# Kernel optimization log

Measured on AMD Instinct MI355X. Metric: run time of the kernel, lower is better.

The kernel has to match this reference:

```python
import jax, jax.numpy as jnp
import numpy as np

HIDDEN = 256
BATCH = 16
SEQ = 8192


def setup_inputs() -> dict:
    key = jax.random.key(0)
    k1, k2 = jax.random.split(key)
    x = jax.random.normal(k1, (BATCH, SEQ, HIDDEN), dtype=jnp.float32)
    # rotor_net parameters: Linear(hidden, hidden) followed by tanh
    W = jax.random.normal(k2, (HIDDEN, HIDDEN), dtype=jnp.float32) / np.sqrt(HIDDEN)
    b = jnp.zeros((HIDDEN,), dtype=jnp.float32)
    return {"x": x, "W": W, "b": b}


def reference(x, W, b):
    # Original torch code loops over subseq_size=10 chunks of the flattened
    # (B*S, H) tokens, applying rotor_net to each chunk and concatenating.
    # rotor_net is row-wise (Linear + tanh), so chunked application is
    # mathematically identical to one batched application over all tokens.
    B, S, H = x.shape
    flat = x.reshape(-1, H)                      # (B*S, H)
    out = jnp.tanh(flat @ W.T + b)               # (B*S, H)
    return out.reshape(B, S, -1)
```

## Files before the change

### kernel.cpp

```cpp
#include <hip/hip_runtime.h>
#include <hip/hip_bf16.h>


#define HIDDEN 256
#define M_TOTAL (16 * 8192)
#define NBLK 512
#define CHUNKS_PER_BLK ((M_TOTAL / 32) / NBLK)

using bf16x8 = __attribute__((ext_vector_type(8))) __bf16;
using bf16x4 = __attribute__((ext_vector_type(4))) __bf16;
using f32x4  = __attribute__((ext_vector_type(4))) float;

__device__ __forceinline__ bf16x4 cvt4(float4 v) {
    bf16x4 r;
    r[0] = (__bf16)v.x; r[1] = (__bf16)v.y;
    r[2] = (__bf16)v.z; r[3] = (__bf16)v.w;
    return r;
}

__global__ __launch_bounds__(256) void wfrag_kernel(const float* __restrict__ W,
                                                    __bf16* __restrict__ WF) {
    const int gid  = blockIdx.x * 256 + threadIdx.x;
    const int lane = gid & 63;
    const int t    = (gid >> 6) & 3;
    const int c    = (gid >> 8) & 7;
    const int nb   = gid >> 11;
    const int lr = lane & 15, q = lane >> 4;
    const float* src = W + (size_t)(nb * 64 + t * 16 + lr) * HIDDEN + c * 32 + q * 8;
    float4 lo = *(const float4*)src;
    float4 hi = *(const float4*)(src + 4);
    bf16x8 v;
    v[0] = (__bf16)lo.x; v[1] = (__bf16)lo.y; v[2] = (__bf16)lo.z; v[3] = (__bf16)lo.w;
    v[4] = (__bf16)hi.x; v[5] = (__bf16)hi.y; v[6] = (__bf16)hi.z; v[7] = (__bf16)hi.w;
    *(bf16x8*)(WF + (size_t)gid * 8) = v;
}

__global__ __launch_bounds__(256, 2) void rotor_kernel(const float* __restrict__ X,
                                                       const __bf16* __restrict__ WF,
                                                       const float* __restrict__ bias,
                                                       float* __restrict__ Y) {
    __shared__ __align__(16) unsigned char lds_raw[2 * 16384 + 4 * 4352];
    __bf16* sXb = (__bf16*)lds_raw;
    float*  sO  = (float*)(lds_raw + 32768 + (threadIdx.x >> 6) * 4352);

    const int tid  = threadIdx.x;
    const int lane = tid & 63;
    const int wave = tid >> 6;
    const int lr = lane & 15, q = lane >> 4;

    const int xrow = tid >> 3;
    const int xc   = tid & 7;
    int woff[8];
#pragma unroll
    for (int j = 0; j < 8; ++j)
        woff[j] = j * 1024 + (xrow >> 4) * 512 + ((xc >> 1) * 16 + (xrow & 15)) * 8 + (xc & 1) * 4;

    const size_t blk_row0 = (size_t)blockIdx.x * (CHUNKS_PER_BLK * 32);
    const float* xbase = X + (blk_row0 + xrow) * HIDDEN + xc * 4;

    float4 xr[8];
#pragma unroll
    for (int j = 0; j < 8; ++j) xr[j] = *(const float4*)(xbase + j * 32);

    const __bf16* wf = WF + (size_t)wave * (8 * 4 * 512) + lane * 8;
    bf16x8 bW[8][4];
#pragma unroll
    for (int c = 0; c < 8; ++c)
#pragma unroll
        for (int t = 0; t < 4; ++t)
            bW[c][t] = *(const bf16x8*)(wf + (c * 4 + t) * 512);

    float bv[4];
#pragma unroll
    for (int t = 0; t < 4; ++t) bv[t] = bias[wave * 64 + t * 16 + lr];

#pragma unroll
    for (int j = 0; j < 8; ++j) *(bf16x4*)(sXb + woff[j]) = cvt4(xr[j]);
    asm volatile("s_waitcnt lgkmcnt(0)" ::: "memory");
    __builtin_amdgcn_s_barrier();
    asm volatile("" ::: "memory");

#pragma unroll 1
    for (int it = 0; it < CHUNKS_PER_BLK; ++it) {
        const int cur = it & 1;

        if (it + 1 < CHUNKS_PER_BLK) {
            const float* xs = xbase + (size_t)(it + 1) * 32 * HIDDEN;
#pragma unroll
            for (int j = 0; j < 8; ++j) xr[j] = *(const float4*)(xs + j * 32);
        }

        f32x4 acc[2][4];
#pragma unroll
        for (int m = 0; m < 2; ++m)
#pragma unroll
            for (int t = 0; t < 4; ++t)
                acc[m][t] = (f32x4){0.f, 0.f, 0.f, 0.f};

        const __bf16* sX = sXb + cur * 8192;
#pragma unroll
        for (int c = 0; c < 8; ++c) {
            const __bf16* ab = sX + c * 1024 + lane * 8;
            bf16x8 a0 = *(const bf16x8*)ab;
            bf16x8 a1 = *(const bf16x8*)(ab + 512);
            acc[0][0] = __builtin_amdgcn_mfma_f32_16x16x32_bf16(a0, bW[c][0], acc[0][0], 0, 0, 0);
            acc[0][1] = __builtin_amdgcn_mfma_f32_16x16x32_bf16(a0, bW[c][1], acc[0][1], 0, 0, 0);
            acc[0][2] = __builtin_amdgcn_mfma_f32_16x16x32_bf16(a0, bW[c][2], acc[0][2], 0, 0, 0);
            acc[0][3] = __builtin_amdgcn_mfma_f32_16x16x32_bf16(a0, bW[c][3], acc[0][3], 0, 0, 0);
            acc[1][0] = __builtin_amdgcn_mfma_f32_16x16x32_bf16(a1, bW[c][0], acc[1][0], 0, 0, 0);
            acc[1][1] = __builtin_amdgcn_mfma_f32_16x16x32_bf16(a1, bW[c][1], acc[1][1], 0, 0, 0);
            acc[1][2] = __builtin_amdgcn_mfma_f32_16x16x32_bf16(a1, bW[c][2], acc[1][2], 0, 0, 0);
            acc[1][3] = __builtin_amdgcn_mfma_f32_16x16x32_bf16(a1, bW[c][3], acc[1][3], 0, 0, 0);
        }

        float* yb = Y + (blk_row0 + (size_t)it * 32) * HIDDEN + wave * 64;
#pragma unroll
        for (int m = 0; m < 2; ++m) {
#pragma unroll
            for (int t = 0; t < 4; ++t)
#pragma unroll
                for (int r = 0; r < 4; ++r) {
                    float z = acc[m][t][r] + bv[t];
                    z = fminf(fmaxf(z, -10.f), 10.f);
                    const float e2 = __expf(2.0f * z);
                    sO[(q * 4 + r) * 68 + t * 16 + lr] = __fdividef(e2 - 1.0f, e2 + 1.0f);
                }
#pragma unroll
            for (int j = 0; j < 4; ++j) {
                f32x4 v = *(const f32x4*)(sO + (j * 4 + q) * 68 + lr * 4);
                __builtin_nontemporal_store(v,
                    (f32x4*)(yb + (size_t)(m * 16 + j * 4 + q) * HIDDEN + lr * 4));
            }
        }

        if (it + 1 < CHUNKS_PER_BLK) {
            __bf16* sW = sXb + (cur ^ 1) * 8192;
#pragma unroll
            for (int j = 0; j < 8; ++j) *(bf16x4*)(sW + woff[j]) = cvt4(xr[j]);
        }
        asm volatile("s_waitcnt lgkmcnt(0)" ::: "memory");
        __builtin_amdgcn_s_barrier();
        asm volatile("" ::: "memory");
    }
}

extern "C" void kernel_launch(void* const* d_in, const int* in_sizes, int n_in,
                              void* d_out, int out_size, void* d_ws, size_t ws_size,
                              hipStream_t stream) {
    const float* X    = (const float*)d_in[0];
    const float* W    = (const float*)d_in[1];
    const float* bias = (const float*)d_in[2];
    float* Y          = (float*)d_out;
    __bf16* WF        = (__bf16*)d_ws;

    wfrag_kernel<<<dim3(32), dim3(256), 0, stream>>>(W, WF);
    rotor_kernel<<<dim3(NBLK), dim3(256), 0, stream>>>(X, WF, bias, Y);
}
```

Before: 246.8 us.

## Stream X into swizzled fp32 LDS via direct global-to-LDS loads, split N across blocks

Rows of X are now copied straight from global memory into a double-buffered, XOR-swizzled fp32 LDS tile with global_load_lds, and converted to bf16 only when MFMA operands are read. Register staging and the separate LDS output transpose go away. Each block now handles 16 rows by 128 output columns, so pairs of blocks share input rows. The grid becomes a grid-stride loop of 768 blocks at occupancy 3. The costs are reading each X row twice (relying on L2 reuse between paired blocks) and writing outputs with scalar nontemporal stores instead of 16-byte vector stores.

After: 249.4 us. Within noise of the previous version (+1.1%).

```diff
diff --git a/kernel.cpp b/kernel.cpp
--- a/kernel.cpp
+++ b/kernel.cpp
@@ -4,18 +4,16 @@
 
 #define HIDDEN 256
 #define M_TOTAL (16 * 8192)
-#define NBLK 512
-#define CHUNKS_PER_BLK ((M_TOTAL / 32) / NBLK)
+#define UNITS 16384
+#define NBLK 768
 
 using bf16x8 = __attribute__((ext_vector_type(8))) __bf16;
-using bf16x4 = __attribute__((ext_vector_type(4))) __bf16;
 using f32x4  = __attribute__((ext_vector_type(4))) float;
 
-__device__ __forceinline__ bf16x4 cvt4(float4 v) {
-    bf16x4 r;
-    r[0] = (__bf16)v.x; r[1] = (__bf16)v.y;
-    r[2] = (__bf16)v.z; r[3] = (__bf16)v.w;
-    return r;
+__device__ __forceinline__ void gload16(const void* g, void* l) {
+    __builtin_amdgcn_global_load_lds(
+        (const __attribute__((address_space(1))) void*)g,
+        (__attribute__((address_space(3))) void*)l, 16, 0, 0);
 }
 
 __global__ __launch_bounds__(256) void wfrag_kernel(const float* __restrict__ W,
@@ -35,112 +33,99 @@
     *(bf16x8*)(WF + (size_t)gid * 8) = v;
 }
 
-__global__ __launch_bounds__(256, 2) void rotor_kernel(const float* __restrict__ X,
+__global__ __launch_bounds__(256, 3) void rotor_kernel(const float* __restrict__ X,
                                                        const __bf16* __restrict__ WF,
                                                        const float* __restrict__ bias,
                                                        float* __restrict__ Y) {
-    __shared__ __align__(16) unsigned char lds_raw[2 * 16384 + 4 * 4352];
-    __bf16* sXb = (__bf16*)lds_raw;
-    float*  sO  = (float*)(lds_raw + 32768 + (threadIdx.x >> 6) * 4352);
+    __shared__ __align__(16) float sX[2][16 * 256];
 
     const int tid  = threadIdx.x;
     const int lane = tid & 63;
     const int wave = tid >> 6;
     const int lr = lane & 15, q = lane >> 4;
+    const int bid = blockIdx.x;
+    const int h   = bid & 1;
 
-    const int xrow = tid >> 3;
-    const int xc   = tid & 7;
-    int woff[8];
-#pragma unroll
-    for (int j = 0; j < 8; ++j)
-        woff[j] = j * 1024 + (xrow >> 4) * 512 + ((xc >> 1) * 16 + (xrow & 15)) * 8 + (xc & 1) * 4;
-
-    const size_t blk_row0 = (size_t)blockIdx.x * (CHUNKS_PER_BLK * 32);
-    const float* xbase = X + (blk_row0 + xrow) * HIDDEN + xc * 4;
-
-    float4 xr[8];
-#pragma unroll
-    for (int j = 0; j < 8; ++j) xr[j] = *(const float4*)(xbase + j * 32);
-
-    const __bf16* wf = WF + (size_t)wave * (8 * 4 * 512) + lane * 8;
-    bf16x8 bW[8][4];
+    const int nb  = h * 2 + (wave >> 1);
+    const int tl0 = (wave & 1) * 2;
+    const __bf16* wf = WF + (size_t)nb * (8 * 4 * 512) + lane * 8;
+    bf16x8 bW[8][2];
 #pragma unroll
     for (int c = 0; c < 8; ++c)
 #pragma unroll
-        for (int t = 0; t < 4; ++t)
-            bW[c][t] = *(const bf16x8*)(wf + (c * 4 + t) * 512);
+        for (int t = 0; t < 2; ++t)
+            bW[c][t] = *(const bf16x8*)(wf + (c * 4 + tl0 + t) * 512);
 
-    float bv[4];
+    float bv[2];
 #pragma unroll
-    for (int t = 0; t < 4; ++t) bv[t] = bias[wave * 64 + t * 16 + lr];
+    for (int t = 0; t < 2; ++t) bv[t] = bias[h * 128 + wave * 32 + t * 16 + lr];
 
+    int srcoff[4];
 #pragma unroll
-    for (int j = 0; j < 8; ++j) *(bf16x4*)(sXb + woff[j]) = cvt4(xr[j]);
-    asm volatile("s_waitcnt lgkmcnt(0)" ::: "memory");
+    for (int k = 0; k < 4; ++k) {
+        const int r = wave * 4 + k;
+        srcoff[k] = (lane * 16) ^ (((r & 7) << 5) | ((r & 8) << 1));
+    }
+    const int swr = ((lr & 7) << 3) | ((lr & 8) >> 1);
+
+    {
+        const int rc = bid >> 1;
+#pragma unroll
+        for (int k = 0; k < 4; ++k)
+            gload16((const char*)X + (size_t)(rc * 16 + wave * 4 + k) * 1024 + srcoff[k],
+                    (char*)&sX[0][(wave * 4 + k) * 256]);
+    }
+    asm volatile("s_waitcnt vmcnt(0)" ::: "memory");
     __builtin_amdgcn_s_barrier();
     asm volatile("" ::: "memory");
 
+    int cur = 0;
 #pragma unroll 1
-    for (int it = 0; it < CHUNKS_PER_BLK; ++it) {
-        const int cur = it & 1;
+    for (int u = bid; u < UNITS; u += NBLK) {
+        const int rc = u >> 1;
 
-        if (it + 1 < CHUNKS_PER_BLK) {
-            const float* xs = xbase + (size_t)(it + 1) * 32 * HIDDEN;
+        const int un = u + NBLK;
+        if (un < UNITS) {
+            const int rcn = un >> 1;
 #pragma unroll
-            for (int j = 0; j < 8; ++j) xr[j] = *(const float4*)(xs + j * 32);
+            for (int k = 0; k < 4; ++k)
+                gload16((const char*)X + (size_t)(rcn * 16 + wave * 4 + k) * 1024 + srcoff[k],
+                        (char*)&sX[cur ^ 1][(wave * 4 + k) * 256]);
         }
 
-        f32x4 acc[2][4];
-#pragma unroll
-        for (int m = 0; m < 2; ++m)
-#pragma unroll
-            for (int t = 0; t < 4; ++t)
-                acc[m][t] = (f32x4){0.f, 0.f, 0.f, 0.f};
-
-        const __bf16* sX = sXb + cur * 8192;
+        const float* sxr = &sX[cur][lr * 256];
+        f32x4 acc0 = {0.f, 0.f, 0.f, 0.f};
+        f32x4 acc1 = {0.f, 0.f, 0.f, 0.f};
 #pragma unroll
         for (int c = 0; c < 8; ++c) {
-            const __bf16* ab = sX + c * 1024 + lane * 8;
-            bf16x8 a0 = *(const bf16x8*)ab;
-            bf16x8 a1 = *(const bf16x8*)(ab + 512);
-            acc[0][0] = __builtin_amdgcn_mfma_f32_16x16x32_bf16(a0, bW[c][0], acc[0][0], 0, 0, 0);
-            acc[0][1] = __builtin_amdgcn_mfma_f32_16x16x32_bf16(a0, bW[c][1], acc[0][1], 0, 0, 0);
-            acc[0][2] = __builtin_amdgcn_mfma_f32_16x16x32_bf16(a0, bW[c][2], acc[0][2], 0, 0, 0);
-            acc[0][3] = __builtin_amdgcn_mfma_f32_16x16x32_bf16(a0, bW[c][3], acc[0][3], 0, 0, 0);
-            acc[1][0] = __builtin_amdgcn_mfma_f32_16x16x32_bf16(a1, bW[c][0], acc[1][0], 0, 0, 0);
-            acc[1][1] = __builtin_amdgcn_mfma_f32_16x16x32_bf16(a1, bW[c][1], acc[1][1], 0, 0, 0);
-            acc[1][2] = __builtin_amdgcn_mfma_f32_16x16x32_bf16(a1, bW[c][2], acc[1][2], 0, 0, 0);
-            acc[1][3] = __builtin_amdgcn_mfma_f32_16x16x32_bf16(a1, bW[c][3], acc[1][3], 0, 0, 0);
+            const int b0 = c * 32 + q * 8;
+            f32x4 lo = *(const f32x4*)(sxr + (b0 ^ swr));
+            f32x4 hi = *(const f32x4*)(sxr + ((b0 + 4) ^ swr));
+            bf16x8 a;
+            a[0] = (__bf16)lo[0]; a[1] = (__bf16)lo[1];
+            a[2] = (__bf16)lo[2]; a[3] = (__bf16)lo[3];
+            a[4] = (__bf16)hi[0]; a[5] = (__bf16)hi[1];
+            a[6] = (__bf16)hi[2]; a[7] = (__bf16)hi[3];
+            acc0 = __builtin_amdgcn_mfma_f32_16x16x32_bf16(a, bW[c][0], acc0, 0, 0, 0);
+            acc1 = __builtin_amdgcn_mfma_f32_16x16x32_bf16(a, bW[c][1], acc1, 0, 0, 0);
         }
 
-        float* yb = Y + (blk_row0 + (size_t)it * 32) * HIDDEN + wave * 64;
+        float* yb = Y + (size_t)(rc * 16 + q * 4) * HIDDEN + h * 128 + wave * 32 + lr;
 #pragma unroll
-        for (int m = 0; m < 2; ++m) {
+        for (int t = 0; t < 2; ++t)
 #pragma unroll
-            for (int t = 0; t < 4; ++t)
-#pragma unroll
-                for (int r = 0; r < 4; ++r) {
-                    float z = acc[m][t][r] + bv[t];
-                    z = fminf(fmaxf(z, -10.f), 10.f);
-                    const float e2 = __expf(2.0f * z);
-                    sO[(q * 4 + r) * 68 + t * 16 + lr] = __fdividef(e2 - 1.0f, e2 + 1.0f);
-                }
-#pragma unroll
-            for (int j = 0; j < 4; ++j) {
-                f32x4 v = *(const f32x4*)(sO + (j * 4 + q) * 68 + lr * 4);
-                __builtin_nontemporal_store(v,
-                    (f32x4*)(yb + (size_t)(m * 16 + j * 4 + q) * HIDDEN + lr * 4));
+            for (int i = 0; i < 4; ++i) {
+                float z = (t ? acc1[i] : acc0[i]) + bv[t];
+                z = fminf(fmaxf(z, -10.f), 10.f);
+                const float e2 = __expf(2.0f * z);
+                __builtin_nontemporal_store(__fdividef(e2 - 1.0f, e2 + 1.0f),
+                                            yb + (size_t)i * HIDDEN + t * 16);
             }
-        }
 
-        if (it + 1 < CHUNKS_PER_BLK) {
-            __bf16* sW = sXb + (cur ^ 1) * 8192;
-#pragma unroll
-            for (int j = 0; j < 8; ++j) *(bf16x4*)(sW + woff[j]) = cvt4(xr[j]);
-        }
-        asm volatile("s_waitcnt lgkmcnt(0)" ::: "memory");
+        asm volatile("s_waitcnt vmcnt(8)" ::: "memory");
         __builtin_amdgcn_s_barrier();
         asm volatile("" ::: "memory");
+        cur ^= 1;
     }
 }
 
```
